# Performance work log

Hardware: AMD Instinct MI355X
Metric: run time of the kernel (lower is better)

The kernel has to match this reference:

```python
import jax, jax.numpy as jnp
import numpy as np

# dims: N batch, O out_channels, CI in_channels, H=W vertices, R rank
N, O, CI, H, R = 8, 32, 16, 512, 8


def setup_inputs() -> dict:
    key = jax.random.key(0)
    kx, kw, kb = jax.random.split(key, 3)
    X = jax.random.normal(kx, (N, CI, H, H), dtype=jnp.float32)
    # learnable left generator (right generator aliases it under symmetry=True)
    weight_L = jax.random.normal(kw, (O, CI, H, R), dtype=jnp.float32) * 0.02
    fan_in = CI * H * R  # torch fan_in for a (O, CI, H, R) weight
    bound = 1.0 / np.sqrt(fan_in)
    bias = jax.random.uniform(kb, (O,), dtype=jnp.float32, minval=-bound, maxval=bound)
    # coupling='split': fixed (non-learnable) +/-1 diagonal coupling, first O//2 channels negative
    coupling = jnp.ones((O, CI, R, 1), dtype=jnp.float32).at[: O // 2].multiply(-1.0)
    return {"X": X, "weight_L": weight_L, "bias": bias, "coupling": coupling}


def reference(X, weight_L, bias, coupling):
    # --- template expansion: T[o,c] = L diag(coupling) L^T  (symmetric, low-rank) ---
    # coupling: (O,CI,R,1) -> per-rank sign broadcast over the rank axis of L
    Lc = weight_L * coupling[..., 0][..., None, :]            # (O,CI,H,R)
    T = jnp.einsum('ochr,ocwr->ochw', Lc, weight_L)           # (O,CI,H,W)
    # --- crosshair similarity, with the in_channel sum pulled inside ---
    P = jnp.einsum('nchw,ochw->nohw', X, T)                   # (N,O,H,W)
    out = P.sum(-1, keepdims=True) + P.sum(-2, keepdims=True) - P
    out = out + bias[None, :, None, None]
    # --- delete diagonal ---
    eye = jnp.eye(out.shape[-1], dtype=out.dtype)
    return out * (1.0 - eye)
```

## Files before the change

### kernel.cpp

```cpp
#include <hip/hip_runtime.h>
#include <cstdint>
#include <cstddef>
#include <utility>

#define Ndim 8
#define Odim 32
#define Cdim 16
#define Hdim 512
#define Rdim 8
#define TW 64
#define TH 4
#define NBW (Hdim/TW)
#define NBH (Hdim/TH)

typedef _Float16 half2_t __attribute__((ext_vector_type(2)));

union U16 { uint4 u; half2_t h[4]; };

template <class F, int... Is>
__device__ __forceinline__ void unroll_impl(F&& f, std::integer_sequence<int, Is...>) {
    (f(std::integral_constant<int, Is>{}), ...);
}
template <int N, class F>
__device__ __forceinline__ void unrollN(F&& f) {
    unroll_impl(static_cast<F&&>(f), std::make_integer_sequence<int, N>{});
}

__device__ __forceinline__ half2_t pk(float a, float b) {
    half2_t h; h[0] = (_Float16)a; h[1] = (_Float16)b; return h;
}

#if defined(__has_builtin)
#if __has_builtin(__builtin_amdgcn_fdot2)
#define HAVE_FDOT2 1
#endif
#endif

__device__ __forceinline__ float fdot2f(half2_t a, half2_t b, float acc) {
#ifdef HAVE_FDOT2
    return __builtin_amdgcn_fdot2(a, b, acc, false);
#else
    return acc + (float)a[0] * (float)b[0] + (float)a[1] * (float)b[1];
#endif
}

__device__ __forceinline__ void stage16(const uint4* g, uint4* l) {
    __builtin_amdgcn_global_load_lds(
        (const __attribute__((address_space(1))) uint32_t*)g,
        (__attribute__((address_space(3))) uint32_t*)l, 16, 0, 0);
}

template<int CTRL>
__device__ __forceinline__ float dppadd(float v) {
    return v + __int_as_float(__builtin_amdgcn_update_dpp(
        0, __float_as_int(v), CTRL, 0xf, 0xf, true));
}
__device__ __forceinline__ float wave_sum63(float v) {
    v = dppadd<0xB1>(v);
    v = dppadd<0x4E>(v);
    v = dppadd<0x141>(v);
    v = dppadd<0x140>(v);
    v = dppadd<0x142>(v);
    v = dppadd<0x143>(v);
    return v;
}

__global__ __launch_bounds__(256)
void sylo_prep(const float* __restrict__ L, const float* __restrict__ coup,
               uint4* __restrict__ lsigT, uint4* __restrict__ lraw)
{
    int row = blockIdx.x * 256 + threadIdx.x;
    int oc = row >> 9, h = row & 511;
    int o = oc >> 4, c = oc & 15;
    const float4* lp = (const float4*)(L + (size_t)row * Rdim);
    const float4* cp = (const float4*)(coup + (size_t)oc * Rdim);
    float4 l0 = lp[0], l1 = lp[1];
    float4 c0 = cp[0], c1 = cp[1];
    U16 s, r;
    s.h[0] = pk(l0.x * c0.x, l0.y * c0.y); s.h[1] = pk(l0.z * c0.z, l0.w * c0.w);
    s.h[2] = pk(l1.x * c1.x, l1.y * c1.y); s.h[3] = pk(l1.z * c1.z, l1.w * c1.w);
    r.h[0] = pk(l0.x, l0.y); r.h[1] = pk(l0.z, l0.w);
    r.h[2] = pk(l1.x, l1.y); r.h[3] = pk(l1.z, l1.w);
    lsigT[((size_t)o * Hdim + h) * Cdim + c] = s.u;
    lraw[row] = r.u;
}

template<int PASS, int MODE>
__global__ __launch_bounds__(256, 3)
void sylo_main(const float* __restrict__ Xg, const float* __restrict__ Lg,
               const float* __restrict__ coupg, const float* __restrict__ biasg,
               const uint4* __restrict__ lsigT, const uint4* __restrict__ lraw,
               float* __restrict__ outg,
               float* __restrict__ rsp, float* __restrict__ csp,
               float* __restrict__ rs, float* __restrict__ cs)
{
    const int tid = threadIdx.x;
    const int j = tid & 63, iw = tid >> 6;
    const int bw = blockIdx.x, bh = blockIdx.y;
    const int w0 = bw * TW, h0 = bh * TH;
    const int hh = h0 + iw;
    const int ww = w0 + j;
    const size_t S = (size_t)Ndim * Odim * Hdim;

    __shared__ __align__(16) uint4 lw[2][Cdim][TW];
    __shared__ float csl[(PASS == 0) ? (2 * TH * Ndim * TW) : 64];

    half2_t xa[64];
    {
        const size_t HH = (size_t)Hdim * Hdim;
        const size_t q = (size_t)hh * Hdim + ww;
        unrollN<8>([&](auto cpi) {
            unrollN<8>([&](auto ni) {
                constexpr int cp = decltype(cpi)::value, n = decltype(ni)::value;
                xa[cp * 8 + n] = pk(Xg[(size_t)(n * Cdim + 2 * cp) * HH + q],
                                    Xg[(size_t)(n * Cdim + 2 * cp + 1) * HH + q]);
            });
        });
    }

    const int ruh = __builtin_amdgcn_readfirstlane(hh);

    if (MODE < 2) {
        unrollN<4>([&](auto ki) {
            constexpr int k = decltype(ki)::value;
            int c = iw * 4 + k;
            stage16(lraw + ((size_t)c * Hdim + w0 + j), &lw[0][c][0]);
        });
        asm volatile("s_waitcnt vmcnt(0)" ::: "memory");
        __builtin_amdgcn_s_barrier();
        __builtin_amdgcn_sched_barrier(0);
    }

    for (int o = 0; o < Odim; ++o) {
        const int cur = (MODE < 2) ? (o & 1) : 0;

        if (MODE < 2) {
            if (o + 1 < Odim) {
                unrollN<4>([&](auto ki) {
                    constexpr int k = decltype(ki)::value;
                    int c = iw * 4 + k;
                    stage16(lraw + ((size_t)((o + 1) * Cdim + c) * Hdim + w0 + j),
                            &lw[cur ^ 1][c][0]);
                });
            }
            __builtin_amdgcn_sched_barrier(0);
        } else {
            __syncthreads();
            unrollN<4>([&](auto ki) {
                constexpr int k = decltype(ki)::value;
                int e = tid + k * 256, c = e >> 6, w = e & 63;
                const float4* gp = (const float4*)(Lg + ((size_t)(o * Cdim + c) * Hdim + w0 + w) * Rdim);
                float4 l0 = gp[0], l1 = gp[1];
                U16 t;
                t.h[0] = pk(l0.x, l0.y); t.h[1] = pk(l0.z, l0.w);
                t.h[2] = pk(l1.x, l1.y); t.h[3] = pk(l1.z, l1.w);
                lw[0][c][w] = t.u;
            });
            __syncthreads();
        }

        half2_t t2[8];
        float tprev = 0.f;
        unrollN<16>([&](auto ci) {
            constexpr int c = decltype(ci)::value;
            U16 A, B;
            if (MODE < 2) {
                A.u = lsigT[((size_t)o * Hdim + ruh) * Cdim + c];
            } else {
                const float4* a0 = (const float4*)(Lg + ((size_t)(o * Cdim + c) * Hdim + ruh) * Rdim);
                const float4* cpp = (const float4*)(coupg + (size_t)(o * Cdim + c) * Rdim);
                float4 l0 = a0[0], l1 = a0[1];
                float4 c0 = cpp[0], c1 = cpp[1];
                A.h[0] = pk(l0.x * c0.x, l0.y * c0.y); A.h[1] = pk(l0.z * c0.z, l0.w * c0.w);
                A.h[2] = pk(l1.x * c1.x, l1.y * c1.y); A.h[3] = pk(l1.z * c1.z, l1.w * c1.w);
            }
            B.u = lw[cur][c][j];
            float t = 0.f;
            unrollN<4>([&](auto ri) {
                constexpr int r = decltype(ri)::value;
                t = fdot2f(A.h[r], B.h[r], t);
            });
            if constexpr (c & 1) t2[c >> 1] = pk(tprev, t);
            else                 tprev = t;
        });

        float p[Ndim];
        unrollN<8>([&](auto ni) { p[decltype(ni)::value] = 0.f; });
        unrollN<8>([&](auto cpi) {
            unrollN<8>([&](auto ni) {
                constexpr int cp = decltype(cpi)::value, n = decltype(ni)::value;
                p[n] = fdot2f(t2[cp], xa[cp * 8 + n], p[n]);
            });
        });

        if (PASS == 0) {
            const int oc = o & 1;
            unrollN<8>([&](auto ni) {
                constexpr int n = decltype(ni)::value;
                float r = wave_sum63(p[n]);
                if (j == 63) {
                    size_t i0 = (size_t)(n * Odim + o) * Hdim + hh;
                    if (MODE == 0) rsp[(size_t)bw * S + i0] = r;
                    else atomicAdd(&rs[i0], r);
                }
                csl[((oc * TH + iw) * Ndim + n) * TW + j] = p[n];
            });
            if (oc == 1) {
                if (MODE < 2) {
                    asm volatile("s_waitcnt lgkmcnt(0)" ::: "memory");
                    __builtin_amdgcn_s_barrier();
                    __builtin_amdgcn_sched_barrier(0);
                } else __syncthreads();
                unrollN<4>([&](auto ki) {
                    constexpr int k = decltype(ki)::value;
                    int f = tid + k * 256;
                    int oo = f >> 9, n = (f >> 6) & 7, jj = f & 63;
                    float v = csl[((oo * TH + 0) * Ndim + n) * TW + jj]
                            + csl[((oo * TH + 1) * Ndim + n) * TW + jj]
                            + csl[((oo * TH + 2) * Ndim + n) * TW + jj]
                            + csl[((oo * TH + 3) * Ndim + n) * TW + jj];
                    size_t idx = (size_t)(n * Odim + (o - 1 + oo)) * Hdim + w0 + jj;
                    if (MODE == 0) csp[(size_t)bh * S + idx] = v;
                    else atomicAdd(&cs[idx], v);
                });
                if (MODE < 2) __builtin_amdgcn_s_barrier();
                else          __syncthreads();
            }
        } else {
            float bb = biasg[o];
            unrollN<8>([&](auto ni) {
                constexpr int n = decltype(ni)::value;
                size_t i0 = (size_t)(n * Odim + o) * Hdim;
                float rv = rs[i0 + (size_t)ruh];
                float cv = cs[i0 + ww];
                float v = rv + cv - p[n] + bb;
                if (hh == ww) v = 0.f;
                outg[(i0 + hh) * Hdim + ww] = v;
            });
        }

        if (MODE < 2) {
            if (PASS == 0) {
                if ((o & 1) == 1) asm volatile("s_waitcnt vmcnt(12)" ::: "memory");
                else              asm volatile("s_waitcnt vmcnt(8)"  ::: "memory");
            } else {
                asm volatile("s_waitcnt vmcnt(16)" ::: "memory");
            }
            __builtin_amdgcn_s_barrier();
            __builtin_amdgcn_sched_barrier(0);
        }
    }
}

__global__ __launch_bounds__(256)
void sylo_reduce(const float* __restrict__ rsp, const float* __restrict__ csp,
                 float* __restrict__ rs, float* __restrict__ cs)
{
    int t = blockIdx.x * 256 + threadIdx.x;
    const size_t S = (size_t)Ndim * Odim * Hdim;
    float a = 0.f;
    #pragma unroll
    for (int k = 0; k < NBW; ++k) a += rsp[(size_t)k * S + t];
    rs[t] = a;
    float b = 0.f;
    #pragma unroll 16
    for (int k = 0; k < NBH; ++k) b += csp[(size_t)k * S + t];
    cs[t] = b;
}

extern "C" void kernel_launch(void* const* d_in, const int* in_sizes, int n_in,
                              void* d_out, int out_size, void* d_ws, size_t ws_size,
                              hipStream_t stream)
{
    const float* X    = (const float*)d_in[0];
    const float* L    = (const float*)d_in[1];
    const float* bias = (const float*)d_in[2];
    const float* coup = (const float*)d_in[3];
    float* out = (float*)d_out;

    const size_t S    = (size_t)Ndim * Odim * Hdim;
    const size_t NL16 = (size_t)Odim * Cdim * Hdim;
    const size_t need0 = NL16 * 16 * 2 + (NBW + NBH + 2) * S * 4;
    const size_t need1 = NL16 * 16 * 2 + 2 * S * 4;
    dim3 grid(NBW, NBH), blk(256);

    if (ws_size >= need0) {
        uint4* lsigT = (uint4*)d_ws;
        uint4* lraw  = lsigT + NL16;
        float* rsp = (float*)(lraw + NL16);
        float* csp = rsp + (size_t)NBW * S;
        float* rs  = csp + (size_t)NBH * S;
        float* cs  = rs + S;
        sylo_prep<<<dim3(1024), blk, 0, stream>>>(L, coup, lsigT, lraw);
        sylo_main<0,0><<<grid, blk, 0, stream>>>(X, L, coup, bias, lsigT, lraw, out, rsp, csp, rs, cs);
        sylo_reduce<<<dim3(512), blk, 0, stream>>>(rsp, csp, rs, cs);
        sylo_main<1,0><<<grid, blk, 0, stream>>>(X, L, coup, bias, lsigT, lraw, out, rsp, csp, rs, cs);
    } else if (ws_size >= need1) {
        uint4* lsigT = (uint4*)d_ws;
        uint4* lraw  = lsigT + NL16;
        float* rs = (float*)(lraw + NL16);
        float* cs = rs + S;
        hipMemsetAsync(rs, 0, 2 * S * sizeof(float), stream);
        sylo_prep<<<dim3(1024), blk, 0, stream>>>(L, coup, lsigT, lraw);
        sylo_main<0,1><<<grid, blk, 0, stream>>>(X, L, coup, bias, lsigT, lraw, out, nullptr, nullptr, rs, cs);
        sylo_main<1,1><<<grid, blk, 0, stream>>>(X, L, coup, bias, lsigT, lraw, out, nullptr, nullptr, rs, cs);
    } else {
        float* rs = (float*)d_ws;
        float* cs = rs + S;
        hipMemsetAsync(rs, 0, 2 * S * sizeof(float), stream);
        sylo_main<0,2><<<grid, blk, 0, stream>>>(X, L, coup, bias, nullptr, nullptr, out, nullptr, nullptr, rs, cs);
        sylo_main<1,2><<<grid, blk, 0, stream>>>(X, L, coup, bias, nullptr, nullptr, out, nullptr, nullptr, rs, cs);
    }
}
```

Before: 312.8 us.

## Split output-channel loop across grid z and interleave T computation with X contraction

Splits the 32 output-channel loop into two halves mapped to a third grid dimension, doubling the block count. Each block now reloads its X tile into registers for only half the channels. The per-channel T dot products are now interleaved with the X contraction to cut live registers, and launch bounds rise to 4 and 5 blocks per CU. The hand-written vmcnt waits and raw s_barrier calls are replaced by plain __syncthreads, which may expose load latency in the double-buffered staging.

Result: slower. 531.7 us (+70.0%).

```diff
diff --git a/kernel.cpp b/kernel.cpp
--- a/kernel.cpp
+++ b/kernel.cpp
@@ -12,6 +12,8 @@
 #define TH 4
 #define NBW (Hdim/TW)
 #define NBH (Hdim/TH)
+#define OSPLIT 2
+#define OPB (Odim/OSPLIT)
 
 typedef _Float16 half2_t __attribute__((ext_vector_type(2)));
 
@@ -85,57 +87,96 @@
     lraw[row] = r.u;
 }
 
-template<int PASS, int MODE>
-__global__ __launch_bounds__(256, 3)
-void sylo_main(const float* __restrict__ Xg, const float* __restrict__ Lg,
-               const float* __restrict__ coupg, const float* __restrict__ biasg,
-               const uint4* __restrict__ lsigT, const uint4* __restrict__ lraw,
-               float* __restrict__ outg,
-               float* __restrict__ rsp, float* __restrict__ csp,
-               float* __restrict__ rs, float* __restrict__ cs)
+template<int MODE>
+__device__ __forceinline__ void compute_p(
+    int o, int ruh, int j, const uint4 (&lwb)[Cdim][TW],
+    const uint4* __restrict__ lsigT, const float* __restrict__ Lg,
+    const float* __restrict__ coupg, const half2_t (&xa)[64], float (&p)[Ndim])
+{
+    unrollN<8>([&](auto ni) { p[decltype(ni)::value] = 0.f; });
+    unrollN<8>([&](auto cpi) {
+        constexpr int cp = decltype(cpi)::value;
+        float tv[2];
+        unrollN<2>([&](auto hi) {
+            constexpr int half = decltype(hi)::value;
+            constexpr int c = 2 * cp + half;
+            U16 A, B;
+            if (MODE < 2) {
+                A.u = lsigT[((size_t)o * Hdim + ruh) * Cdim + c];
+            } else {
+                const float4* a0 = (const float4*)(Lg + ((size_t)(o * Cdim + c) * Hdim + ruh) * Rdim);
+                const float4* cpp = (const float4*)(coupg + (size_t)(o * Cdim + c) * Rdim);
+                float4 l0 = a0[0], l1 = a0[1];
+                float4 c0 = cpp[0], c1 = cpp[1];
+                A.h[0] = pk(l0.x * c0.x, l0.y * c0.y); A.h[1] = pk(l0.z * c0.z, l0.w * c0.w);
+                A.h[2] = pk(l1.x * c1.x, l1.y * c1.y); A.h[3] = pk(l1.z * c1.z, l1.w * c1.w);
+            }
+            B.u = lwb[c][j];
+            float t = 0.f;
+            unrollN<4>([&](auto ri) {
+                constexpr int r = decltype(ri)::value;
+                t = fdot2f(A.h[r], B.h[r], t);
+            });
+            tv[half] = t;
+        });
+        half2_t t2 = pk(tv[0], tv[1]);
+        unrollN<8>([&](auto ni) {
+            constexpr int n = decltype(ni)::value;
+            p[n] = fdot2f(t2, xa[cp * 8 + n], p[n]);
+        });
+    });
+}
+
+#define X_PROLOGUE                                                              \
+    half2_t xa[64];                                                             \
+    {                                                                           \
+        const size_t HH = (size_t)Hdim * Hdim;                                  \
+        const size_t q = (size_t)hh * Hdim + ww;                                \
+        unrollN<8>([&](auto cpi) {                                              \
+            unrollN<8>([&](auto ni) {                                           \
+                constexpr int cp = decltype(cpi)::value, n = decltype(ni)::value;\
+                xa[cp * 8 + n] = pk(Xg[(size_t)(n * Cdim + 2 * cp) * HH + q],   \
+                                    Xg[(size_t)(n * Cdim + 2 * cp + 1) * HH + q]);\
+            });                                                                 \
+        });                                                                     \
+    }
+
+template<int MODE>
+__global__ __launch_bounds__(256, 4)
+void sylo_p0(const float* __restrict__ Xg, const float* __restrict__ Lg,
+             const float* __restrict__ coupg,
+             const uint4* __restrict__ lsigT, const uint4* __restrict__ lraw,
+             float* __restrict__ rsp, float* __restrict__ csp,
+             float* __restrict__ rs, float* __restrict__ cs)
 {
     const int tid = threadIdx.x;
     const int j = tid & 63, iw = tid >> 6;
-    const int bw = blockIdx.x, bh = blockIdx.y;
+    const int bw = blockIdx.x, bh = blockIdx.y, ob = blockIdx.z * OPB;
     const int w0 = bw * TW, h0 = bh * TH;
-    const int hh = h0 + iw;
-    const int ww = w0 + j;
+    const int hh = h0 + iw, ww = w0 + j;
     const size_t S = (size_t)Ndim * Odim * Hdim;
 
     __shared__ __align__(16) uint4 lw[2][Cdim][TW];
-    __shared__ float csl[(PASS == 0) ? (2 * TH * Ndim * TW) : 64];
-
-    half2_t xa[64];
-    {
-        const size_t HH = (size_t)Hdim * Hdim;
-        const size_t q = (size_t)hh * Hdim + ww;
-        unrollN<8>([&](auto cpi) {
-            unrollN<8>([&](auto ni) {
-                constexpr int cp = decltype(cpi)::value, n = decltype(ni)::value;
-                xa[cp * 8 + n] = pk(Xg[(size_t)(n * Cdim + 2 * cp) * HH + q],
-                                    Xg[(size_t)(n * Cdim + 2 * cp + 1) * HH + q]);
-            });
-        });
-    }
-
+    __shared__ float csl[TH][Ndim][TW];
+
+    X_PROLOGUE
     const int ruh = __builtin_amdgcn_readfirstlane(hh);
 
     if (MODE < 2) {
         unrollN<4>([&](auto ki) {
             constexpr int k = decltype(ki)::value;
             int c = iw * 4 + k;
-            stage16(lraw + ((size_t)c * Hdim + w0 + j), &lw[0][c][0]);
-        });
-        asm volatile("s_waitcnt vmcnt(0)" ::: "memory");
-        __builtin_amdgcn_s_barrier();
-        __builtin_amdgcn_sched_barrier(0);
-    }
-
-    for (int o = 0; o < Odim; ++o) {
-        const int cur = (MODE < 2) ? (o & 1) : 0;
+            stage16(lraw + ((size_t)(ob * Cdim + c) * Hdim + w0 + j), &lw[0][c][0]);
+        });
+    }
+    __syncthreads();
+
+    for (int oo = 0; oo < OPB; ++oo) {
+        const int o = ob + oo;
+        const int cur = (MODE < 2) ? (oo & 1) : 0;
 
         if (MODE < 2) {
-            if (o + 1 < Odim) {
+            if (oo + 1 < OPB) {
                 unrollN<4>([&](auto ki) {
                     constexpr int k = decltype(ki)::value;
                     int c = iw * 4 + k;
@@ -143,9 +184,7 @@
                             &lw[cur ^ 1][c][0]);
                 });
             }
-            __builtin_amdgcn_sched_barrier(0);
         } else {
-            __syncthreads();
             unrollN<4>([&](auto ki) {
                 constexpr int k = decltype(ki)::value;
                 int e = tid + k * 256, c = e >> 6, w = e & 63;
@@ -159,96 +198,102 @@
             __syncthreads();
         }
 
-        half2_t t2[8];
-        float tprev = 0.f;
-        unrollN<16>([&](auto ci) {
-            constexpr int c = decltype(ci)::value;
-            U16 A, B;
-            if (MODE < 2) {
-                A.u = lsigT[((size_t)o * Hdim + ruh) * Cdim + c];
-            } else {
-                const float4* a0 = (const float4*)(Lg + ((size_t)(o * Cdim + c) * Hdim + ruh) * Rdim);
-                const float4* cpp = (const float4*)(coupg + (size_t)(o * Cdim + c) * Rdim);
-                float4 l0 = a0[0], l1 = a0[1];
-                float4 c0 = cpp[0], c1 = cpp[1];
-                A.h[0] = pk(l0.x * c0.x, l0.y * c0.y); A.h[1] = pk(l0.z * c0.z, l0.w * c0.w);
-                A.h[2] = pk(l1.x * c1.x, l1.y * c1.y); A.h[3] = pk(l1.z * c1.z, l1.w * c1.w);
+        float p[Ndim];
+        compute_p<MODE>(o, ruh, j, lw[cur], lsigT, Lg, coupg, xa, p);
+
+        unrollN<8>([&](auto ni) {
+            constexpr int n = decltype(ni)::value;
+            float r = wave_sum63(p[n]);
+            if (j == 63) {
+                size_t i0 = (size_t)(n * Odim + o) * Hdim + hh;
+                if (MODE == 0) rsp[(size_t)bw * S + i0] = r;
+                else atomicAdd(&rs[i0], r);
             }
-            B.u = lw[cur][c][j];
-            float t = 0.f;
-            unrollN<4>([&](auto ri) {
-                constexpr int r = decltype(ri)::value;
-                t = fdot2f(A.h[r], B.h[r], t);
-            });
-            if constexpr (c & 1) t2[c >> 1] = pk(tprev, t);
-            else                 tprev = t;
-        });
-
-        float p[Ndim];
-        unrollN<8>([&](auto ni) { p[decltype(ni)::value] = 0.f; });
-        unrollN<8>([&](auto cpi) {
-            unrollN<8>([&](auto ni) {
-                constexpr int cp = decltype(cpi)::value, n = decltype(ni)::value;
-                p[n] = fdot2f(t2[cp], xa[cp * 8 + n], p[n]);
-            });
-        });
-
-        if (PASS == 0) {
-            const int oc = o & 1;
-            unrollN<8>([&](auto ni) {
-                constexpr int n = decltype(ni)::value;
-                float r = wave_sum63(p[n]);
-                if (j == 63) {
-                    size_t i0 = (size_t)(n * Odim + o) * Hdim + hh;
-                    if (MODE == 0) rsp[(size_t)bw * S + i0] = r;
-                    else atomicAdd(&rs[i0], r);
-                }
-                csl[((oc * TH + iw) * Ndim + n) * TW + j] = p[n];
-            });
-            if (oc == 1) {
-                if (MODE < 2) {
-                    asm volatile("s_waitcnt lgkmcnt(0)" ::: "memory");
-                    __builtin_amdgcn_s_barrier();
-                    __builtin_amdgcn_sched_barrier(0);
-                } else __syncthreads();
+            csl[iw][n][j] = p[n];
+        });
+        __syncthreads();
+        unrollN<2>([&](auto ki) {
+            constexpr int k = decltype(ki)::value;
+            int f = tid + k * 256;
+            int n = f >> 6, jj = f & 63;
+            float v = csl[0][n][jj] + csl[1][n][jj] + csl[2][n][jj] + csl[3][n][jj];
+            size_t idx = (size_t)(n * Odim + o) * Hdim + w0 + jj;
+            if (MODE == 0) csp[(size_t)bh * S + idx] = v;
+            else atomicAdd(&cs[idx], v);
+        });
+        __syncthreads();
+    }
+}
+
+template<int MODE>
+__global__ __launch_bounds__(256, 5)
+void sylo_p1(const float* __restrict__ Xg, const float* __restrict__ Lg,
+             const float* __restrict__ coupg, const float* __restrict__ biasg,
+             const uint4* __restrict__ lsigT, const uint4* __restrict__ lraw,
+             float* __restrict__ outg,
+             const float* __restrict__ rs, const float* __restrict__ cs)
+{
+    const int tid = threadIdx.x;
+    const int j = tid & 63, iw = tid >> 6;
+    const int bw = blockIdx.x, bh = blockIdx.y, ob = blockIdx.z * OPB;
+    const int w0 = bw * TW, h0 = bh * TH;
+    const int hh = h0 + iw, ww = w0 + j;
+
+    __shared__ __align__(16) uint4 lw[2][Cdim][TW];
+
+    X_PROLOGUE
+    const int ruh = __builtin_amdgcn_readfirstlane(hh);
+
+    if (MODE < 2) {
+        unrollN<4>([&](auto ki) {
+            constexpr int k = decltype(ki)::value;
+            int c = iw * 4 + k;
+            stage16(lraw + ((size_t)(ob * Cdim + c) * Hdim + w0 + j), &lw[0][c][0]);
+        });
+    }
+    __syncthreads();
+
+    for (int oo = 0; oo < OPB; ++oo) {
+        const int o = ob + oo;
+        const int cur = (MODE < 2) ? (oo & 1) : 0;
+
+        if (MODE < 2) {
+            if (oo + 1 < OPB) {
                 unrollN<4>([&](auto ki) {
                     constexpr int k = decltype(ki)::value;
-                    int f = tid + k * 256;
-                    int oo = f >> 9, n = (f >> 6) & 7, jj = f & 63;
-                    float v = csl[((oo * TH + 0) * Ndim + n) * TW + jj]
-                            + csl[((oo * TH + 1) * Ndim + n) * TW + jj]
-                            + csl[((oo * TH + 2) * Ndim + n) * TW + jj]
-                            + csl[((oo * TH + 3) * Ndim + n) * TW + jj];
-                    size_t idx = (size_t)(n * Odim + (o - 1 + oo)) * Hdim + w0 + jj;
-                    if (MODE == 0) csp[(size_t)bh * S + idx] = v;
-                    else atomicAdd(&cs[idx], v);
+                    int c = iw * 4 + k;
+                    stage16(lraw + ((size_t)((o + 1) * Cdim + c) * Hdim + w0 + j),
+                            &lw[cur ^ 1][c][0]);
                 });
-                if (MODE < 2) __builtin_amdgcn_s_barrier();
-                else          __syncthreads();
             }
         } else {
-            float bb = biasg[o];
-            unrollN<8>([&](auto ni) {
-                constexpr int n = decltype(ni)::value;
-                size_t i0 = (size_t)(n * Odim + o) * Hdim;
-                float rv = rs[i0 + (size_t)ruh];
-                float cv = cs[i0 + ww];
-                float v = rv + cv - p[n] + bb;
-                if (hh == ww) v = 0.f;
-                outg[(i0 + hh) * Hdim + ww] = v;
+            unrollN<4>([&](auto ki) {
+                constexpr int k = decltype(ki)::value;
+                int e = tid + k * 256, c = e >> 6, w = e & 63;
+                const float4* gp = (const float4*)(Lg + ((size_t)(o * Cdim + c) * Hdim + w0 + w) * Rdim);
+                float4 l0 = gp[0], l1 = gp[1];
+                U16 t;
+                t.h[0] = pk(l0.x, l0.y); t.h[1] = pk(l0.z, l0.w);
+                t.h[2] = pk(l1.x, l1.y); t.h[3] = pk(l1.z, l1.w);
+                lw[0][c][w] = t.u;
             });
+            __syncthreads();
         }
 
-        if (MODE < 2) {
-            if (PASS == 0) {
-                if ((o & 1) == 1) asm volatile("s_waitcnt vmcnt(12)" ::: "memory");
-                else              asm volatile("s_waitcnt vmcnt(8)"  ::: "memory");
-            } else {
-                asm volatile("s_waitcnt vmcnt(16)" ::: "memory");
-            }
-            __builtin_amdgcn_s_barrier();
-            __builtin_amdgcn_sched_barrier(0);
-        }
+        float p[Ndim];
+        compute_p<MODE>(o, ruh, j, lw[cur], lsigT, Lg, coupg, xa, p);
+
+        float bb = biasg[o];
+        unrollN<8>([&](auto ni) {
+            constexpr int n = decltype(ni)::value;
+            size_t i0 = (size_t)(n * Odim + o) * Hdim;
+            float rv = rs[i0 + (size_t)ruh];
+            float cv = cs[i0 + ww];
+            float v = rv + cv - p[n] + bb;
+            if (hh == ww) v = 0.f;
+            outg[(i0 + hh) * Hdim + ww] = v;
+        });
+        __syncthreads();
     }
 }
 
@@ -282,7 +327,7 @@
     const size_t NL16 = (size_t)Odim * Cdim * Hdim;
     const size_t need0 = NL16 * 16 * 2 + (NBW + NBH + 2) * S * 4;
     const size_t need1 = NL16 * 16 * 2 + 2 * S * 4;
-    dim3 grid(NBW, NBH), blk(256);
+    dim3 grid(NBW, NBH, OSPLIT), blk(256);
 
     if (ws_size >= need0) {
         uint4* lsigT = (uint4*)d_ws;
@@ -292,9 +337,9 @@
         float* rs  = csp + (size_t)NBH * S;
         float* cs  = rs + S;
         sylo_prep<<<dim3(1024), blk, 0, stream>>>(L, coup, lsigT, lraw);
-        sylo_main<0,0><<<grid, blk, 0, stream>>>(X, L, coup, bias, lsigT, lraw, out, rsp, csp, rs, cs);
+        sylo_p0<0><<<grid, blk, 0, stream>>>(X, L, coup, lsigT, lraw, rsp, csp, rs, cs);
         sylo_reduce<<<dim3(512), blk, 0, stream>>>(rsp, csp, rs, cs);
-        sylo_main<1,0><<<grid, blk, 0, stream>>>(X, L, coup, bias, lsigT, lraw, out, rsp, csp, rs, cs);
+        sylo_p1<0><<<grid, blk, 0, stream>>>(X, L, coup, bias, lsigT, lraw, out, rs, cs);
     } else if (ws_size >= need1) {
         uint4* lsigT = (uint4*)d_ws;
         uint4* lraw  = lsigT + NL16;
@@ -302,13 +347,13 @@
         float* cs = rs + S;
         hipMemsetAsync(rs, 0, 2 * S * sizeof(float), stream);
         sylo_prep<<<dim3(1024), blk, 0, stream>>>(L, coup, lsigT, lraw);
-        sylo_main<0,1><<<grid, blk, 0, stream>>>(X, L, coup, bias, lsigT, lraw, out, nullptr, nullptr, rs, cs);
-        sylo_main<1,1><<<grid, blk, 0, stream>>>(X, L, coup, bias, lsigT, lraw, out, nullptr, nullptr, rs, cs);
+        sylo_p0<1><<<grid, blk, 0, stream>>>(X, L, coup, lsigT, lraw, nullptr, nullptr, rs, cs);
+        sylo_p1<1><<<grid, blk, 0, stream>>>(X, L, coup, bias, lsigT, lraw, out, rs, cs);
     } else {
         float* rs = (float*)d_ws;
         float* cs = rs + S;
         hipMemsetAsync(rs, 0, 2 * S * sizeof(float), stream);
-        sylo_main<0,2><<<grid, blk, 0, stream>>>(X, L, coup, bias, nullptr, nullptr, out, nullptr, nullptr, rs, cs);
-        sylo_main<1,2><<<grid, blk, 0, stream>>>(X, L, coup, bias, nullptr, nullptr, out, nullptr, nullptr, rs, cs);
-    }
-}
+        sylo_p0<2><<<grid, blk, 0, stream>>>(X, L, coup, nullptr, nullptr, nullptr, nullptr, rs, cs);
+        sylo_p1<2><<<grid, blk, 0, stream>>>(X, L, coup, bias, nullptr, nullptr, out, rs, cs);
+    }
+}
```
